# Kernel optimization log

Hardware: AMD Instinct MI355X
Metric: run time of the kernel (lower is better)

The kernel has to match this reference:

```python
import jax
import jax.numpy as jnp
import numpy as np

TOKENS, D_IN, D_OUT = 8192, 4096, 4096
QMAX = 127.0


def setup_inputs() -> dict:
    key = jax.random.key(0)
    k_x, k_w, k_s, k_o, k_b = jax.random.split(key, 5)
    x = jax.random.normal(k_x, (TOKENS, D_IN), dtype=jnp.float32)
    # int8-valued weight stored as int32 for portability (values in [-127, 127])
    weight = jax.random.randint(k_w, (D_OUT, D_IN), -127, 128, dtype=jnp.int32)
    # realistic small per-channel dequant scales
    weight_scale = (jax.random.uniform(k_s, (D_OUT,), dtype=jnp.float32) + 0.5) * 0.01
    # module stores -weight_offset; keep small integer-ish zero points
    weight_offset = jnp.round(jax.random.normal(k_o, (D_OUT,), dtype=jnp.float32) * 4.0)
    bias = jax.random.normal(k_b, (D_OUT,), dtype=jnp.float32) * 0.1
    return {"x": x, "weight": weight, "weight_scale": weight_scale,
            "weight_offset": weight_offset, "bias": bias}


def reference(x, weight, weight_scale, weight_offset, bias):
    # --- dynamic per-token symmetric activation quantization ---
    act_scale = jnp.max(jnp.abs(x), axis=-1, keepdims=True) / QMAX   # [T, 1]
    x_q = jnp.clip(jnp.round(x / act_scale), -QMAX, QMAX)            # int-valued fp32 [T, D_in]

    # --- int8 GEMM with per-channel zero-point correction ---
    # stored weight_offset = -zero_point, so dequant weight = scale * (w_q + weight_offset)
    acc = x_q @ weight.astype(jnp.float32).T                          # [T, D_out]
    zp_corr = jnp.sum(x_q, axis=-1, keepdims=True) * weight_offset[None, :]
    acc = acc + zp_corr

    # --- dequant + bias epilogue ---
    y = acc * act_scale * weight_scale[None, :] + bias[None, :]
    return y
```

## Files before the change

### kernel.cpp

```cpp
#include <hip/hip_runtime.h>
#include <cstdint>
#include <cstddef>

#define TOKENS 8192
#define DIN    4096
#define DOUT   4096

typedef int int4v  __attribute__((ext_vector_type(4)));
typedef int int16v __attribute__((ext_vector_type(16)));

__global__ __launch_bounds__(256) void quant_rows(const float* __restrict__ x,
                                                  int* __restrict__ xq,
                                                  float* __restrict__ ascale,
                                                  int* __restrict__ rsum) {
  const int row = blockIdx.x;
  const int t = threadIdx.x;
  const float4* xr = (const float4*)(x + (size_t)row * DIN);
  float4 v[4];
#pragma unroll
  for (int i = 0; i < 4; ++i) v[i] = xr[i * 256 + t];

  float m = 0.f;
#pragma unroll
  for (int i = 0; i < 4; ++i) {
    m = fmaxf(m, fabsf(v[i].x)); m = fmaxf(m, fabsf(v[i].y));
    m = fmaxf(m, fabsf(v[i].z)); m = fmaxf(m, fabsf(v[i].w));
  }
#pragma unroll
  for (int off = 32; off; off >>= 1) m = fmaxf(m, __shfl_xor(m, off));

  __shared__ float wmax[4];
  __shared__ int   wsum[4];
  const int lane = t & 63, wid = t >> 6;
  if (lane == 0) wmax[wid] = m;
  __syncthreads();
  m = fmaxf(fmaxf(wmax[0], wmax[1]), fmaxf(wmax[2], wmax[3]));

  const float s = m * (1.0f / 127.0f);
  const float sdiv = (m > 0.f) ? s : 1.0f;

  int ssum = 0;
#pragma unroll
  for (int i = 0; i < 4; ++i) {
    float q;
    q = fminf(fmaxf(rintf(v[i].x / sdiv), -127.f), 127.f); const int b0 = (int)q;
    q = fminf(fmaxf(rintf(v[i].y / sdiv), -127.f), 127.f); const int b1 = (int)q;
    q = fminf(fmaxf(rintf(v[i].z / sdiv), -127.f), 127.f); const int b2 = (int)q;
    q = fminf(fmaxf(rintf(v[i].w / sdiv), -127.f), 127.f); const int b3 = (int)q;
    ssum += b0 + b1 + b2 + b3;
    xq[(size_t)row * 1024 + i * 256 + t] =
        (b0 & 255) | ((b1 & 255) << 8) | ((b2 & 255) << 16) | ((b3 & 255) << 24);
  }
#pragma unroll
  for (int off = 32; off; off >>= 1) ssum += __shfl_xor(ssum, off);
  if (lane == 0) wsum[wid] = ssum;
  __syncthreads();
  if (t == 0) {
    rsum[row]   = wsum[0] + wsum[1] + wsum[2] + wsum[3];
    ascale[row] = s;
  }
}

__global__ __launch_bounds__(256) void wconv(const int* __restrict__ w,
                                             int* __restrict__ w8) {
  const int idx = blockIdx.x * 256 + threadIdx.x;
  const int4 v = ((const int4*)w)[idx];
  w8[idx] = (v.x & 255) | ((v.y & 255) << 8) | ((v.z & 255) << 16) | ((v.w & 255) << 24);
}

#define GLOAD(G_, L_) __builtin_amdgcn_global_load_lds(                       \
      (const __attribute__((address_space(1))) void*)(G_),                    \
      (__attribute__((address_space(3))) void*)(L_), 16, 0, 0)

#define RD(AV_, BV_, L_, AO_, BO_)                                            \
    _Pragma("unroll")                                                         \
    for (int mi = 0; mi < 4; ++mi)                                            \
      AV_[mi] = *(const int4v*)((L_) + (AO_) + mi * 2048);                    \
    _Pragma("unroll")                                                         \
    for (int ni = 0; ni < 2; ++ni)                                            \
      BV_[ni] = *(const int4v*)((L_) + (BO_) + ni * 2048);

#define MFMA8(AV_, BV_)                                                       \
  __builtin_amdgcn_s_setprio(1);                                              \
  _Pragma("unroll")                                                           \
  for (int mi = 0; mi < 4; ++mi) {                                            \
    acc[mi][0] = __builtin_amdgcn_mfma_i32_32x32x32_i8(AV_[mi], BV_[0], acc[mi][0], 0, 0, 0); \
    acc[mi][1] = __builtin_amdgcn_mfma_i32_32x32x32_i8(AV_[mi], BV_[1], acc[mi][1], 0, 0, 0); \
  }                                                                           \
  __builtin_amdgcn_s_setprio(0);

#define SUPER(S_, STG_, BAR_)                                                 \
  do {                                                                        \
    if (STG_) {                                                               \
      char* W2 = lds + (((S_) + 2) & 3) * 32768;                              \
      char* W3 = lds + (((S_) + 3) & 3) * 32768;                              \
      const size_t k2 = (size_t)((S_) + 2) * 64;                              \
      const size_t k3 = (size_t)((S_) + 3) * 64;                              \
      GLOAD(gA0 + k2, W2 + ldst);                                             \
      GLOAD(gA1 + k2, W2 + 8192 + ldst);                                      \
      GLOAD(gB0 + k2, W2 + 16384 + ldst);                                     \
      GLOAD(gB1 + k2, W2 + 24576 + ldst);                                     \
      GLOAD(gA0 + k3, W3 + ldst);                                             \
      GLOAD(gA1 + k3, W3 + 8192 + ldst);                                      \
      GLOAD(gB0 + k3, W3 + 16384 + ldst);                                     \
      GLOAD(gB1 + k3, W3 + 24576 + ldst);                                     \
    }                                                                         \
    {                                                                         \
      const char* L0 = lds + ((S_) & 3) * 32768;                              \
      const char* L1 = lds + (((S_) + 1) & 3) * 32768;                        \
      RD(aB, bB, L0, aoff1, boff1)                               \
      MFMA8(aA, bA)                                              \
      RD(aA, bA, L1, aoff0, boff0)                               \
      MFMA8(aB, bB)                                              \
      RD(aB, bB, L1, aoff1, boff1)                               \
      MFMA8(aA, bA)                                              \
      MFMA8(aB, bB)                                              \
    }                                                                         \
    if (BAR_) {                                                               \
      asm volatile("s_waitcnt vmcnt(0)" ::: "memory");                        \
      __builtin_amdgcn_s_barrier();                                           \
      __builtin_amdgcn_sched_barrier(0);                                      \
      const char* L2 = lds + (((S_) + 2) & 3) * 32768;                        \
      RD(aA, bA, L2, aoff0, boff0)                               \
    }                                                                         \
  } while (0)

__global__ __launch_bounds__(512, 2) void gemm_i8(
    const char* __restrict__ xq, const char* __restrict__ w8,
    const float* __restrict__ ascale, const int* __restrict__ rsum,
    const float* __restrict__ wscale, const float* __restrict__ woff,
    const float* __restrict__ bias, float* __restrict__ y) {

  __shared__ __align__(16) char lds[131072];

  const int bid = blockIdx.x;
  const int tm = bid >> 4;
  const int tn = bid & 15;
  const int t = threadIdx.x;
  const int lane = t & 63, wid = t >> 6;
  const int wmI = wid >> 2;
  const int wnI = wid & 3;

  const int S_ = (t * 16) ^ (((t >> 3) & 3) << 4) ^ (((t >> 6) & 1) << 6);
  const int srow = S_ >> 6;
  const int scol = S_ & 63;

  const char* gA0 = xq + (size_t)(tm * 256 + srow) * DIN + scol;
  const char* gA1 = gA0 + (size_t)128 * DIN;
  const char* gB0 = w8 + (size_t)(tn * 256 + srow) * DIN + scol;
  const char* gB1 = gB0 + (size_t)128 * DIN;
  const int ldst = t * 16;

  const int mask  = (((lane >> 1) & 3) << 4) ^ (((lane >> 4) & 1) << 6);
  const int arow  = (lane & 31) * 64 + (lane >> 5) * 16;
  const int aoff0 = wmI * 8192 + ((arow +  0) ^ mask);
  const int aoff1 = wmI * 8192 + ((arow + 32) ^ mask);
  const int brow  = (wnI & 1) * 4096 + arow;
  const int boff0 = (2 + (wnI >> 1)) * 8192 + ((brow +  0) ^ mask);
  const int boff1 = (2 + (wnI >> 1)) * 8192 + ((brow + 32) ^ mask);

  int16v acc[4][2];
#pragma unroll
  for (int mi = 0; mi < 4; ++mi)
#pragma unroll
    for (int ni = 0; ni < 2; ++ni)
#pragma unroll
      for (int rg = 0; rg < 16; ++rg) acc[mi][ni][rg] = 0;

  int4v aA[4], aB[4], bA[2], bB[2];

#pragma unroll
  for (int p = 0; p < 4; ++p) {
    char* Wb = lds + p * 32768;
    GLOAD(gA0 + p * 64, Wb + ldst);
    GLOAD(gA1 + p * 64, Wb + 8192 + ldst);
    GLOAD(gB0 + p * 64, Wb + 16384 + ldst);
    GLOAD(gB1 + p * 64, Wb + 24576 + ldst);
  }
  asm volatile("s_waitcnt vmcnt(8)" ::: "memory");
  __builtin_amdgcn_s_barrier();
  __builtin_amdgcn_sched_barrier(0);
  RD(aA, bA, lds, aoff0, boff0)

  SUPER(0, 0, 1);
  for (int S = 2; S <= 60; S += 2)
    SUPER(S, 1, 1);
  SUPER(62, 0, 0);

  const int rb0 = tm * 256 + wmI * 128 + 4 * (lane >> 5);
  const int cb0 = tn * 256 + wnI * 64 + (lane & 31);
  const float ws0 = wscale[cb0],      ws1 = wscale[cb0 + 32];
  const float wo0 = woff[cb0],        wo1 = woff[cb0 + 32];
  const float bi0 = bias[cb0],        bi1 = bias[cb0 + 32];
#pragma unroll
  for (int mi = 0; mi < 4; ++mi) {
#pragma unroll
    for (int rg = 0; rg < 16; ++rg) {
      const int r = rb0 + mi * 32 + (rg & 3) + 8 * (rg >> 2);
      const float as_ = ascale[r];
      const float rs_ = (float)rsum[r];
      y[(size_t)r * DOUT + cb0]      = ((float)acc[mi][0][rg] + rs_ * wo0) * (as_ * ws0) + bi0;
      y[(size_t)r * DOUT + cb0 + 32] = ((float)acc[mi][1][rg] + rs_ * wo1) * (as_ * ws1) + bi1;
    }
  }
}

extern "C" void kernel_launch(void* const* d_in, const int* in_sizes, int n_in,
                              void* d_out, int out_size, void* d_ws, size_t ws_size,
                              hipStream_t stream) {
  const float* x      = (const float*)d_in[0];
  const int*   w      = (const int*)  d_in[1];
  const float* wscale = (const float*)d_in[2];
  const float* woff   = (const float*)d_in[3];
  const float* bias   = (const float*)d_in[4];
  float* y = (float*)d_out;

  char* ws = (char*)d_ws;
  char*  xq     = ws;
  char*  w8     = ws + (size_t)TOKENS * DIN;
  float* ascale = (float*)(w8 + (size_t)DOUT * DIN);
  int*   rsum   = (int*)(ascale + TOKENS);

  hipLaunchKernelGGL(quant_rows, dim3(TOKENS), dim3(256), 0, stream,
                     x, (int*)xq, ascale, rsum);
  hipLaunchKernelGGL(wconv, dim3((DOUT * DIN / 4) / 256), dim3(256), 0, stream,
                     w, (int*)w8);
  hipLaunchKernelGGL(gemm_i8, dim3((TOKENS / 256) * (DOUT / 256)), dim3(512), 0, stream,
                     xq, w8, ascale, rsum, wscale, woff, bias, y);
}
```

Before: 203.0 us.

## Use 4 waves per block with 128x128 warp tiles instead of 8 waves

Cuts the GEMM block from 512 to 256 threads, so each wave now computes a 128x128 output tile with 4x4 MFMA accumulators instead of 4x2. Global-to-LDS staging is rewritten so each thread issues eight 16-byte loads per k-step to cover the same 256x256 block tile. The aim is more register-level reuse of A/B fragments per LDS read and fewer waves contending for LDS. In exchange, accumulator register pressure doubles and occupancy falls to one block per CU, which leaves fewer waves to hide latency.

Result: slower. 217.7 us (+7.3%).

```diff
diff --git a/kernel.cpp b/kernel.cpp
--- a/kernel.cpp
+++ b/kernel.cpp
@@ -72,49 +72,51 @@
       (const __attribute__((address_space(1))) void*)(G_),                    \
       (__attribute__((address_space(3))) void*)(L_), 16, 0, 0)
 
+#define STAGE(TT_)                                                            \
+  do {                                                                        \
+    char* Wb_ = lds + ((TT_) & 3) * 32768;                                    \
+    const size_t k_ = (size_t)(TT_) * 64;                                     \
+    GLOAD(pA + k_,            Wb_ + ldst);                                    \
+    GLOAD(pA + 64*DIN  + k_,  Wb_ + 4096  + ldst);                            \
+    GLOAD(pA + 128*DIN + k_,  Wb_ + 8192  + ldst);                            \
+    GLOAD(pA + 192*DIN + k_,  Wb_ + 12288 + ldst);                            \
+    GLOAD(pB + k_,            Wb_ + 16384 + ldst);                            \
+    GLOAD(pB + 64*DIN  + k_,  Wb_ + 20480 + ldst);                            \
+    GLOAD(pB + 128*DIN + k_,  Wb_ + 24576 + ldst);                            \
+    GLOAD(pB + 192*DIN + k_,  Wb_ + 28672 + ldst);                            \
+  } while (0)
+
 #define RD(AV_, BV_, L_, AO_, BO_)                                            \
     _Pragma("unroll")                                                         \
     for (int mi = 0; mi < 4; ++mi)                                            \
       AV_[mi] = *(const int4v*)((L_) + (AO_) + mi * 2048);                    \
     _Pragma("unroll")                                                         \
-    for (int ni = 0; ni < 2; ++ni)                                            \
+    for (int ni = 0; ni < 4; ++ni)                                            \
       BV_[ni] = *(const int4v*)((L_) + (BO_) + ni * 2048);
 
-#define MFMA8(AV_, BV_)                                                       \
+#define MFMA16(AV_, BV_)                                                      \
   __builtin_amdgcn_s_setprio(1);                                              \
   _Pragma("unroll")                                                           \
-  for (int mi = 0; mi < 4; ++mi) {                                            \
-    acc[mi][0] = __builtin_amdgcn_mfma_i32_32x32x32_i8(AV_[mi], BV_[0], acc[mi][0], 0, 0, 0); \
-    acc[mi][1] = __builtin_amdgcn_mfma_i32_32x32x32_i8(AV_[mi], BV_[1], acc[mi][1], 0, 0, 0); \
-  }                                                                           \
+  for (int mi = 0; mi < 4; ++mi)                                              \
+    _Pragma("unroll")                                                         \
+    for (int ni = 0; ni < 4; ++ni)                                            \
+      acc[mi][ni] = __builtin_amdgcn_mfma_i32_32x32x32_i8(                    \
+          AV_[mi], BV_[ni], acc[mi][ni], 0, 0, 0);                            \
   __builtin_amdgcn_s_setprio(0);
 
 #define SUPER(S_, STG_, BAR_)                                                 \
   do {                                                                        \
-    if (STG_) {                                                               \
-      char* W2 = lds + (((S_) + 2) & 3) * 32768;                              \
-      char* W3 = lds + (((S_) + 3) & 3) * 32768;                              \
-      const size_t k2 = (size_t)((S_) + 2) * 64;                              \
-      const size_t k3 = (size_t)((S_) + 3) * 64;                              \
-      GLOAD(gA0 + k2, W2 + ldst);                                             \
-      GLOAD(gA1 + k2, W2 + 8192 + ldst);                                      \
-      GLOAD(gB0 + k2, W2 + 16384 + ldst);                                     \
-      GLOAD(gB1 + k2, W2 + 24576 + ldst);                                     \
-      GLOAD(gA0 + k3, W3 + ldst);                                             \
-      GLOAD(gA1 + k3, W3 + 8192 + ldst);                                      \
-      GLOAD(gB0 + k3, W3 + 16384 + ldst);                                     \
-      GLOAD(gB1 + k3, W3 + 24576 + ldst);                                     \
-    }                                                                         \
+    if (STG_) { STAGE((S_) + 2); STAGE((S_) + 3); }                           \
     {                                                                         \
       const char* L0 = lds + ((S_) & 3) * 32768;                              \
       const char* L1 = lds + (((S_) + 1) & 3) * 32768;                        \
       RD(aB, bB, L0, aoff1, boff1)                               \
-      MFMA8(aA, bA)                                              \
+      MFMA16(aA, bA)                                             \
       RD(aA, bA, L1, aoff0, boff0)                               \
-      MFMA8(aB, bB)                                              \
+      MFMA16(aB, bB)                                             \
       RD(aB, bB, L1, aoff1, boff1)                               \
-      MFMA8(aA, bA)                                              \
-      MFMA8(aB, bB)                                              \
+      MFMA16(aA, bA)                                             \
+      MFMA16(aB, bB)                                             \
     }                                                                         \
     if (BAR_) {                                                               \
       asm volatile("s_waitcnt vmcnt(0)" ::: "memory");                        \
@@ -125,7 +127,7 @@
     }                                                                         \
   } while (0)
 
-__global__ __launch_bounds__(512, 2) void gemm_i8(
+__global__ __launch_bounds__(256, 1) void gemm_i8(
     const char* __restrict__ xq, const char* __restrict__ w8,
     const float* __restrict__ ascale, const int* __restrict__ rsum,
     const float* __restrict__ wscale, const float* __restrict__ woff,
@@ -138,46 +140,36 @@
   const int tn = bid & 15;
   const int t = threadIdx.x;
   const int lane = t & 63, wid = t >> 6;
-  const int wmI = wid >> 2;
-  const int wnI = wid & 3;
+  const int wmI = wid >> 1;
+  const int wnI = wid & 1;
 
   const int S_ = (t * 16) ^ (((t >> 3) & 3) << 4) ^ (((t >> 6) & 1) << 6);
   const int srow = S_ >> 6;
   const int scol = S_ & 63;
 
-  const char* gA0 = xq + (size_t)(tm * 256 + srow) * DIN + scol;
-  const char* gA1 = gA0 + (size_t)128 * DIN;
-  const char* gB0 = w8 + (size_t)(tn * 256 + srow) * DIN + scol;
-  const char* gB1 = gB0 + (size_t)128 * DIN;
+  const char* pA = xq + (size_t)(tm * 256 + srow) * DIN + scol;
+  const char* pB = w8 + (size_t)(tn * 256 + srow) * DIN + scol;
   const int ldst = t * 16;
 
   const int mask  = (((lane >> 1) & 3) << 4) ^ (((lane >> 4) & 1) << 6);
   const int arow  = (lane & 31) * 64 + (lane >> 5) * 16;
   const int aoff0 = wmI * 8192 + ((arow +  0) ^ mask);
   const int aoff1 = wmI * 8192 + ((arow + 32) ^ mask);
-  const int brow  = (wnI & 1) * 4096 + arow;
-  const int boff0 = (2 + (wnI >> 1)) * 8192 + ((brow +  0) ^ mask);
-  const int boff1 = (2 + (wnI >> 1)) * 8192 + ((brow + 32) ^ mask);
-
-  int16v acc[4][2];
+  const int boff0 = (2 + wnI) * 8192 + ((arow +  0) ^ mask);
+  const int boff1 = (2 + wnI) * 8192 + ((arow + 32) ^ mask);
+
+  int16v acc[4][4];
 #pragma unroll
   for (int mi = 0; mi < 4; ++mi)
 #pragma unroll
-    for (int ni = 0; ni < 2; ++ni)
+    for (int ni = 0; ni < 4; ++ni)
 #pragma unroll
       for (int rg = 0; rg < 16; ++rg) acc[mi][ni][rg] = 0;
 
-  int4v aA[4], aB[4], bA[2], bB[2];
-
-#pragma unroll
-  for (int p = 0; p < 4; ++p) {
-    char* Wb = lds + p * 32768;
-    GLOAD(gA0 + p * 64, Wb + ldst);
-    GLOAD(gA1 + p * 64, Wb + 8192 + ldst);
-    GLOAD(gB0 + p * 64, Wb + 16384 + ldst);
-    GLOAD(gB1 + p * 64, Wb + 24576 + ldst);
-  }
-  asm volatile("s_waitcnt vmcnt(8)" ::: "memory");
+  int4v aA[4], aB[4], bA[4], bB[4];
+
+  STAGE(0); STAGE(1); STAGE(2); STAGE(3);
+  asm volatile("s_waitcnt vmcnt(16)" ::: "memory");
   __builtin_amdgcn_s_barrier();
   __builtin_amdgcn_sched_barrier(0);
   RD(aA, bA, lds, aoff0, boff0)
@@ -188,10 +180,14 @@
   SUPER(62, 0, 0);
 
   const int rb0 = tm * 256 + wmI * 128 + 4 * (lane >> 5);
-  const int cb0 = tn * 256 + wnI * 64 + (lane & 31);
-  const float ws0 = wscale[cb0],      ws1 = wscale[cb0 + 32];
-  const float wo0 = woff[cb0],        wo1 = woff[cb0 + 32];
-  const float bi0 = bias[cb0],        bi1 = bias[cb0 + 32];
+  const int cb0 = tn * 256 + wnI * 128 + (lane & 31);
+  float ws_[4], wo_[4], bi_[4];
+#pragma unroll
+  for (int ni = 0; ni < 4; ++ni) {
+    ws_[ni] = wscale[cb0 + ni * 32];
+    wo_[ni] = woff[cb0 + ni * 32];
+    bi_[ni] = bias[cb0 + ni * 32];
+  }
 #pragma unroll
   for (int mi = 0; mi < 4; ++mi) {
 #pragma unroll
@@ -199,8 +195,10 @@
       const int r = rb0 + mi * 32 + (rg & 3) + 8 * (rg >> 2);
       const float as_ = ascale[r];
       const float rs_ = (float)rsum[r];
-      y[(size_t)r * DOUT + cb0]      = ((float)acc[mi][0][rg] + rs_ * wo0) * (as_ * ws0) + bi0;
-      y[(size_t)r * DOUT + cb0 + 32] = ((float)acc[mi][1][rg] + rs_ * wo1) * (as_ * ws1) + bi1;
+      float* yr = y + (size_t)r * DOUT + cb0;
+#pragma unroll
+      for (int ni = 0; ni < 4; ++ni)
+        yr[ni * 32] = ((float)acc[mi][ni][rg] + rs_ * wo_[ni]) * (as_ * ws_[ni]) + bi_[ni];
     }
   }
 }
@@ -225,6 +223,6 @@
                      x, (int*)xq, ascale, rsum);
   hipLaunchKernelGGL(wconv, dim3((DOUT * DIN / 4) / 256), dim3(256), 0, stream,
                      w, (int*)w8);
-  hipLaunchKernelGGL(gemm_i8, dim3((TOKENS / 256) * (DOUT / 256)), dim3(512), 0, stream,
+  hipLaunchKernelGGL(gemm_i8, dim3((TOKENS / 256) * (DOUT / 256)), dim3(256), 0, stream,
                      xq, w8, ascale, rsum, wscale, woff, bias, y);
 }
```
